# Kernel tuning notes

Measured on AMD Instinct MI355X. Metric: run time of the kernel, lower is better.

Reference implementation:

```python
import jax, jax.numpy as jnp
import numpy as np

B, T, D = 2, 2048, 1024
H, RANK = 16, 32
DH = D // H  # 64


def setup_inputs() -> dict:
    key = jax.random.key(0)
    ks = jax.random.split(key, 6)
    sd = 1.0 / np.sqrt(D)
    sdh = 1.0 / np.sqrt(DH)
    return {
        "x": jax.random.normal(ks[0], (B, T, D), dtype=jnp.float32),
        "W_qkv": jax.random.normal(ks[1], (D, 3 * D), dtype=jnp.float32) * sd,
        "W_q_lsr": jax.random.normal(ks[2], (H, DH, RANK), dtype=jnp.float32) * sdh,
        "W_k_lsr": jax.random.normal(ks[3], (H, DH, RANK), dtype=jnp.float32) * sdh,
        "lsr_core": jnp.ones((H, RANK), dtype=jnp.float32),
        "W_o": jax.random.normal(ks[4], (D, D), dtype=jnp.float32) * sd,
    }


def reference(x, W_qkv, W_q_lsr, W_k_lsr, lsr_core, W_o):
    b, t, d = x.shape
    # Fused QKV projection
    qkv = x @ W_qkv  # (B, T, 3D)
    q, k, v = jnp.split(qkv, 3, axis=-1)
    # (B, H, T, DH)
    q = q.reshape(b, t, H, DH).transpose(0, 2, 1, 3)
    k = k.reshape(b, t, H, DH).transpose(0, 2, 1, 3)
    v = v.reshape(b, t, H, DH).transpose(0, 2, 1, 3)
    # Low-rank bilinear score: q^T Wq diag(core) Wk^T k
    ql = jnp.einsum("bhtd,hdr->bhtr", q, W_q_lsr)  # (B, H, T, R)
    kl = jnp.einsum("bhsd,hdr->bhsr", k, W_k_lsr)  # (B, H, T, R)
    scale = 1.0 / jnp.sqrt(jnp.asarray(RANK, dtype=x.dtype))
    scores = jnp.einsum("bhtr,bhsr->bhts", ql * lsr_core[None, :, None, :], kl) * scale
    # Causal mask
    causal = jnp.tril(jnp.ones((t, t), dtype=bool))
    scores = jnp.where(causal[None, None], scores, jnp.asarray(-jnp.inf, dtype=scores.dtype))
    attn = jax.nn.softmax(scores, axis=-1)
    y = jnp.einsum("bhts,bhsd->bhtd", attn, v)  # (B, H, T, DH)
    y = y.transpose(0, 2, 1, 3).reshape(b, t, d)
    return y @ W_o
```

## Files before the change

kernel.cpp:

```cpp
#include <hip/hip_runtime.h>
#include <hip/hip_bf16.h>

#define B_  2
#define T_  2048
#define D_  1024
#define H_  16
#define DH_ 64
#define R_  32
#define BT_ (B_*T_)
#define BH_ (B_*H_)

typedef unsigned short u16;
typedef unsigned int   u32;
typedef __attribute__((ext_vector_type(8))) short bhalf8;
typedef __attribute__((ext_vector_type(4))) float floatx4;

#define WSB_FLAG  0
#define WSB_XB    256
#define WSB_WCATT (WSB_XB    + 8388608)
#define WSB_QL    (WSB_WCATT + 4194304)
#define WSB_KL    (WSB_QL    + 4194304)
#define WSB_VT    (WSB_KL    + 4194304)
#define WSB_YB    (WSB_VT    + 8388608)
#define WSB_WOT   (WSB_YB    + 8388608)

#define NEG_ -1.0e30f

__device__ __forceinline__ float bfs(u16 s) {
    union { u32 i; float f; } w; w.i = ((u32)s) << 16; return w.f;
}
__device__ __forceinline__ u16 tob(float f) {
    __hip_bfloat16 h = __float2bfloat16(f);
    return *(u16*)&h;
}
__device__ __forceinline__ u32 pack2(float a, float b) {
    return (u32)tob(a) | ((u32)tob(b) << 16);
}

__global__ __launch_bounds__(64) void detect_dtype(const u32* __restrict__ xw,
                                                   int* __restrict__ flag)
{
    const int tid = threadIdx.x;
    int hits = 0;
    for (int i = tid; i < 512; i += 64) {
        const u32 w = xw[i];
        const u32 h = w & 0xFFFFu;
        const u32 e = (h >> 7) & 0xFFu;
        if (h == 0u || (e >= 100u && e <= 150u)) ++hits;
    }
    #pragma unroll
    for (int off = 32; off; off >>= 1) hits += __shfl_down(hits, off, 64);
    if (tid == 0) *flag = (hits >= 300) ? 1 : 0;
}

__global__ __launch_bounds__(256) void convert_x(
    const void* __restrict__ x, u16* __restrict__ xb,
    const int* __restrict__ flag)
{
    const int isbf = *flag;
    const int e = blockIdx.x * 256 + threadIdx.x;
    if (isbf) {
        ((uint4*)xb)[e] = ((const uint4*)x)[e];
    } else {
        float4 a0 = ((const float4*)x)[2*e];
        float4 a1 = ((const float4*)x)[2*e + 1];
        uint4 o;
        o.x = pack2(a0.x, a0.y); o.y = pack2(a0.z, a0.w);
        o.z = pack2(a1.x, a1.y); o.w = pack2(a1.z, a1.w);
        ((uint4*)xb)[e] = o;
    }
}

__global__ __launch_bounds__(256) void fold_mfma(
    const void* __restrict__ Wqkv, const void* __restrict__ Wq_lsr,
    const void* __restrict__ Wk_lsr, const void* __restrict__ core,
    u16* __restrict__ WcatT, const int* __restrict__ flag)
{
    __shared__ __align__(16) u16 Bq[128 * 72];
    __shared__ __align__(16) u16 Bk[128 * 72];
    __shared__ __align__(16) u16 Aq[32 * 72];
    __shared__ __align__(16) u16 Ak[32 * 72];
    const int isbf = *flag;
    const int tid  = threadIdx.x;
    const int lane = tid & 63;
    const int w    = tid >> 6;
    const int n16  = lane & 15;
    const int q4   = lane >> 4;
    const int h    = blockIdx.y;
    const int d0   = blockIdx.x * 128;

    #pragma unroll
    for (int p = 0; p < 8; ++p) {
        const int e  = tid + p * 256;
        const int r  = e & 31, dh = e >> 5;
        float aq, ak;
        if (isbf) {
            aq = bfs(((const u16*)Wq_lsr)[(h*DH_ + dh)*R_ + r]);
            ak = bfs(((const u16*)Wk_lsr)[(h*DH_ + dh)*R_ + r]);
        } else {
            aq = ((const float*)Wq_lsr)[(h*DH_ + dh)*R_ + r];
            ak = ((const float*)Wk_lsr)[(h*DH_ + dh)*R_ + r];
        }
        Aq[r * 72 + dh] = tob(aq);
        Ak[r * 72 + dh] = tob(ak);
    }
    #pragma unroll
    for (int p = 0; p < 8; ++p) {
        const int e  = tid + p * 256;
        const int n  = e >> 4, ch = e & 15;
        if (isbf) {
            uint2 wq = *(const uint2*)((const u16*)Wqkv + (size_t)(d0+n)*(3*D_) + h*DH_ + ch*4);
            uint2 wk = *(const uint2*)((const u16*)Wqkv + (size_t)(d0+n)*(3*D_) + D_ + h*DH_ + ch*4);
            *(uint2*)&Bq[n * 72 + ch*4] = wq;
            *(uint2*)&Bk[n * 72 + ch*4] = wk;
        } else {
            float4 fq = *(const float4*)((const float*)Wqkv + (size_t)(d0+n)*(3*D_) + h*DH_ + ch*4);
            float4 fk = *(const float4*)((const float*)Wqkv + (size_t)(d0+n)*(3*D_) + D_ + h*DH_ + ch*4);
            uint2 oq, ok;
            oq.x = pack2(fq.x, fq.y); oq.y = pack2(fq.z, fq.w);
            ok.x = pack2(fk.x, fk.y); ok.y = pack2(fk.z, fk.w);
            *(uint2*)&Bq[n * 72 + ch*4] = oq;
            *(uint2*)&Bk[n * 72 + ch*4] = ok;
        }
    }
    __syncthreads();

    floatx4 accq[2][2], acck[2][2];
    #pragma unroll
    for (int mi = 0; mi < 2; ++mi)
        #pragma unroll
        for (int ni = 0; ni < 2; ++ni) { accq[mi][ni] = (floatx4)(0.f); acck[mi][ni] = (floatx4)(0.f); }

    #pragma unroll
    for (int kk = 0; kk < 2; ++kk) {
        bhalf8 aqf[2], akf[2], bqf[2], bkf[2];
        #pragma unroll
        for (int mi = 0; mi < 2; ++mi) {
            aqf[mi] = *(const bhalf8*)&Aq[(mi*16 + n16) * 72 + kk*32 + q4*8];
            akf[mi] = *(const bhalf8*)&Ak[(mi*16 + n16) * 72 + kk*32 + q4*8];
        }
        #pragma unroll
        for (int ni = 0; ni < 2; ++ni) {
            bqf[ni] = *(const bhalf8*)&Bq[(w*32 + ni*16 + n16) * 72 + kk*32 + q4*8];
            bkf[ni] = *(const bhalf8*)&Bk[(w*32 + ni*16 + n16) * 72 + kk*32 + q4*8];
        }
        #pragma unroll
        for (int mi = 0; mi < 2; ++mi)
            #pragma unroll
            for (int ni = 0; ni < 2; ++ni) {
                accq[mi][ni] = __builtin_amdgcn_mfma_f32_16x16x32_bf16(aqf[mi], bqf[ni], accq[mi][ni], 0, 0, 0);
                acck[mi][ni] = __builtin_amdgcn_mfma_f32_16x16x32_bf16(akf[mi], bkf[ni], acck[mi][ni], 0, 0, 0);
            }
    }

    const float scale = (float)(0.17677669529663687 * 1.4426950408889634);
    #pragma unroll
    for (int mi = 0; mi < 2; ++mi) {
        #pragma unroll
        for (int rr = 0; rr < 4; ++rr) {
            const int r = mi*16 + q4*4 + rr;
            const float cc = (isbf ? bfs(((const u16*)core)[h*R_ + r])
                                   : ((const float*)core)[h*R_ + r]) * scale;
            #pragma unroll
            for (int ni = 0; ni < 2; ++ni) {
                const int d = d0 + w*32 + ni*16 + n16;
                WcatT[(size_t)(h*R_ + r) * D_ + d]       = tob(accq[mi][ni][rr] * cc);
                WcatT[(size_t)(512 + h*R_ + r) * D_ + d] = tob(acck[mi][ni][rr]);
            }
        }
    }
}

__global__ __launch_bounds__(256) void convert_T(
    const void* __restrict__ src, u16* __restrict__ dst,
    int srcStride, int srcColOff, int dstRowOff, const int* __restrict__ flag)
{
    __shared__ __align__(16) u16 tile[64 * 72];
    const int isbf = *flag;
    const int tid = threadIdx.x;
    const int j0  = blockIdx.x * 64;
    const int i0  = blockIdx.y * 64;
    #pragma unroll
    for (int p = 0; p < 2; ++p) {
        const int e = tid + p * 256;
        const int r = e >> 3, ch = e & 7;
        if (isbf) {
            uint4 w = *(const uint4*)((const u16*)src + (size_t)(i0 + r) * srcStride + srcColOff + j0 + ch*8);
            *(uint4*)&tile[r * 72 + ch*8] = w;
        } else {
            const float* s = (const float*)src + (size_t)(i0 + r) * srcStride + srcColOff + j0 + ch*8;
            float4 a0 = *(const float4*)s;
            float4 a1 = *(const float4*)(s + 4);
            uint4 o;
            o.x = pack2(a0.x, a0.y); o.y = pack2(a0.z, a0.w);
            o.z = pack2(a1.x, a1.y); o.w = pack2(a1.z, a1.w);
            *(uint4*)&tile[r * 72 + ch*8] = o;
        }
    }
    __syncthreads();
    #pragma unroll
    for (int p = 0; p < 2; ++p) {
        const int e = tid + p * 256;
        const int c = e >> 3, ch = e & 7;
        u16 tmp[8];
        #pragma unroll
        for (int j = 0; j < 8; ++j) tmp[j] = tile[(ch*8 + j) * 72 + c];
        *(uint4*)(dst + (size_t)(dstRowOff + j0 + c) * D_ + i0 + ch*8) = *(uint4*)tmp;
    }
}

__global__ __launch_bounds__(256) void gemm1_mfma(
    const u16* __restrict__ xb, const u16* __restrict__ WcatT,
    u16* __restrict__ ql, u16* __restrict__ kl, u16* __restrict__ v_t)
{
    __shared__ __align__(16) u16 As[128 * 72];
    __shared__ __align__(16) u16 Bs[64 * 72];
    const int tid  = threadIdx.x;
    const int lane = tid & 63;
    const int w    = tid >> 6;
    const int n16  = lane & 15;
    const int q4   = lane >> 4;
    const int wx   = w & 1;
    const int wy   = w >> 1;
    const int bm   = blockIdx.y * 128;
    const int bn   = blockIdx.x * 64;

    floatx4 acc[4][2];
    #pragma unroll
    for (int i = 0; i < 4; ++i)
        #pragma unroll
        for (int j = 0; j < 2; ++j) acc[i][j] = (floatx4)(0.f);

    for (int kt = 0; kt < D_; kt += 64) {
        #pragma unroll
        for (int p = 0; p < 4; ++p) {
            const int e = tid + p * 256;
            const int r = e >> 3, ch = (e & 7) * 8;
            *(uint4*)&As[r * 72 + ch] = *(const uint4*)(xb + (size_t)(bm + r) * D_ + kt + ch);
        }
        #pragma unroll
        for (int p = 0; p < 2; ++p) {
            const int e = tid + p * 256;
            const int r = e >> 3, ch = (e & 7) * 8;
            *(uint4*)&Bs[r * 72 + ch] = *(const uint4*)(WcatT + (size_t)(bn + r) * D_ + kt + ch);
        }
        __syncthreads();
        #pragma unroll
        for (int kk = 0; kk < 2; ++kk) {
            bhalf8 a[4], b[2];
            #pragma unroll
            for (int mi = 0; mi < 4; ++mi)
                a[mi] = *(const bhalf8*)&As[(wy*64 + mi*16 + n16) * 72 + kk*32 + q4*8];
            #pragma unroll
            for (int ni = 0; ni < 2; ++ni)
                b[ni] = *(const bhalf8*)&Bs[(wx*32 + ni*16 + n16) * 72 + kk*32 + q4*8];
            #pragma unroll
            for (int mi = 0; mi < 4; ++mi)
                #pragma unroll
                for (int ni = 0; ni < 2; ++ni)
                    acc[mi][ni] = __builtin_amdgcn_mfma_f32_16x16x32_bf16(
                        a[mi], b[ni], acc[mi][ni], 0, 0, 0);
        }
        __syncthreads();
    }

    if (bn < 1024) {
        #pragma unroll
        for (int mi = 0; mi < 4; ++mi) {
            #pragma unroll
            for (int rr = 0; rr < 4; ++rr) {
                const int row = bm + wy*64 + mi*16 + q4*4 + rr;
                const int b   = row >> 11;
                const int t   = row & (T_ - 1);
                #pragma unroll
                for (int ni = 0; ni < 2; ++ni) {
                    const int col = bn + wx*32 + ni*16 + n16;
                    const u16 val = tob(acc[mi][ni][rr]);
                    if (col < 512) {
                        const int h = col >> 5, r = col & 31;
                        ql[((size_t)(b*H_ + h)*T_ + t)*R_ + r] = val;
                    } else {
                        const int c = col - 512; const int h = c >> 5, r = c & 31;
                        kl[((size_t)(b*H_ + h)*T_ + t)*R_ + r] = val;
                    }
                }
            }
        }
    } else {
        #pragma unroll
        for (int mi = 0; mi < 4; ++mi) {
            const int row0 = bm + wy*64 + mi*16 + q4*4;
            const int b = row0 >> 11;
            const int t = row0 & (T_ - 1);
            #pragma unroll
            for (int ni = 0; ni < 2; ++ni) {
                const int c = bn - 1024 + wx*32 + ni*16 + n16;
                const int h = c >> 6, dh = c & 63;
                uint2 o;
                o.x = pack2(acc[mi][ni][0], acc[mi][ni][1]);
                o.y = pack2(acc[mi][ni][2], acc[mi][ni][3]);
                *(uint2*)(v_t + ((size_t)(b*H_ + h) * DH_ + dh) * T_ + t) = o;
            }
        }
    }
}

__global__ __launch_bounds__(256, 3) void attn_kernel(
    const u16* __restrict__ ql, const u16* __restrict__ kl,
    const u16* __restrict__ v_t, u16* __restrict__ y)
{
    __shared__ __align__(16) u16 kls[128 * 40];
    __shared__ __align__(16) u16 vsT[64 * 136];
    __shared__ __align__(16) u16 Ps [4][16][144];

    const int tid  = threadIdx.x;
    const int lane = tid & 63;
    const int w    = tid >> 6;
    const int n16  = lane & 15;
    const int q4   = lane >> 4;
    const int bh   = blockIdx.x;
    const int qt   = 31 - (int)blockIdx.y;
    const int t0   = qt * 64;
    const int nt   = (qt + 2) >> 1;

    const u16* qlb = ql + (size_t)bh * T_ * R_;
    const bhalf8 aq = *(const bhalf8*)(qlb + (size_t)(t0 + w*16 + n16) * R_ + q4*8);

    const u16* klb = kl  + (size_t)bh * T_ * R_;
    const u16* vtb = v_t + (size_t)bh * DH_ * T_;
    const int rk = tid >> 2, ck = (tid & 3) * 8;
    const int dv = tid >> 4, cv = (tid & 15) * 8;

    uint4 kc0 = *(const uint4*)(klb + (size_t)(rk     ) * R_ + ck);
    uint4 kc1 = *(const uint4*)(klb + (size_t)(rk + 64) * R_ + ck);
    uint4 vc0 = *(const uint4*)(vtb + (size_t)(dv     ) * T_ + cv);
    uint4 vc1 = *(const uint4*)(vtb + (size_t)(dv + 16) * T_ + cv);
    uint4 vc2 = *(const uint4*)(vtb + (size_t)(dv + 32) * T_ + cv);
    uint4 vc3 = *(const uint4*)(vtb + (size_t)(dv + 48) * T_ + cv);
    uint4 kn0 = kc0, kn1 = kc1, vn0 = vc0, vn1 = vc1, vn2 = vc2, vn3 = vc3;

    float mrow = NEG_, lrow = 0.f;
    floatx4 O[4];
    #pragma unroll
    for (int c = 0; c < 4; ++c) O[c] = (floatx4)(0.f);

    for (int it = 0; it < nt; ++it) {
        const int s0 = it * 128;
        __syncthreads();
        *(uint4*)&kls[(rk     ) * 40 + ck] = kc0;
        *(uint4*)&kls[(rk + 64) * 40 + ck] = kc1;
        *(uint4*)&vsT[(dv     ) * 136 + cv] = vc0;
        *(uint4*)&vsT[(dv + 16) * 136 + cv] = vc1;
        *(uint4*)&vsT[(dv + 32) * 136 + cv] = vc2;
        *(uint4*)&vsT[(dv + 48) * 136 + cv] = vc3;
        if (it + 1 < nt) {
            const int s1 = s0 + 128;
            kn0 = *(const uint4*)(klb + (size_t)(s1 + rk     ) * R_ + ck);
            kn1 = *(const uint4*)(klb + (size_t)(s1 + rk + 64) * R_ + ck);
            vn0 = *(const uint4*)(vtb + (size_t)(dv     ) * T_ + s1 + cv);
            vn1 = *(const uint4*)(vtb + (size_t)(dv + 16) * T_ + s1 + cv);
            vn2 = *(const uint4*)(vtb + (size_t)(dv + 32) * T_ + s1 + cv);
            vn3 = *(const uint4*)(vtb + (size_t)(dv + 48) * T_ + s1 + cv);
        }
        __syncthreads();

        floatx4 Sc[8];
        #pragma unroll
        for (int c = 0; c < 8; ++c) {
            bhalf8 ak = *(const bhalf8*)&kls[(16*c + n16) * 40 + q4*8];
            Sc[c] = __builtin_amdgcn_mfma_f32_16x16x32_bf16(ak, aq, (floatx4)(0.f), 0, 0, 0);
        }

        if (it == nt - 1) {
            const int tq = w*16 + n16;
            #pragma unroll
            for (int c = 0; c < 8; ++c) {
                const int sb = s0 - t0 + 16*c + 4*q4;
                #pragma unroll
                for (int r = 0; r < 4; ++r)
                    if (sb + r > tq) Sc[c][r] = NEG_;
            }
        }

        float cmax[8];
        #pragma unroll
        for (int c = 0; c < 8; ++c)
            cmax[c] = fmaxf(fmaxf(Sc[c][0], Sc[c][1]), fmaxf(Sc[c][2], Sc[c][3]));
        float rmax = fmaxf(fmaxf(fmaxf(cmax[0], cmax[1]), fmaxf(cmax[2], cmax[3])),
                           fmaxf(fmaxf(cmax[4], cmax[5]), fmaxf(cmax[6], cmax[7])));
        rmax = fmaxf(rmax, __shfl_xor(rmax, 16, 64));
        rmax = fmaxf(rmax, __shfl_xor(rmax, 32, 64));

        const float mn = fmaxf(mrow, rmax);
        const int norescale = __all(rmax <= mrow);

        float csum[8];
        #pragma unroll
        for (int c = 0; c < 8; ++c) {
            #pragma unroll
            for (int r = 0; r < 4; ++r)
                Sc[c][r] = __builtin_amdgcn_exp2f(Sc[c][r] - mn);
            csum[c] = (Sc[c][0] + Sc[c][1]) + (Sc[c][2] + Sc[c][3]);
        }
        float rsum = ((csum[0] + csum[1]) + (csum[2] + csum[3]))
                   + ((csum[4] + csum[5]) + (csum[6] + csum[7]));
        rsum += __shfl_xor(rsum, 16, 64);
        rsum += __shfl_xor(rsum, 32, 64);

        if (norescale) {
            lrow += rsum;
        } else {
            const float alpha = __builtin_amdgcn_exp2f(mrow - mn);
            mrow = mn;
            lrow = lrow * alpha + rsum;
            float aO[4];
            #pragma unroll
            for (int r = 0; r < 4; ++r) aO[r] = __shfl(alpha, q4*4 + r, 64);
            #pragma unroll
            for (int c2 = 0; c2 < 4; ++c2)
                #pragma unroll
                for (int r = 0; r < 4; ++r) O[c2][r] *= aO[r];
        }

        #pragma unroll
        for (int c = 0; c < 8; ++c) {
            uint2 pw;
            pw.x = pack2(Sc[c][0], Sc[c][1]);
            pw.y = pack2(Sc[c][2], Sc[c][3]);
            *(uint2*)&Ps[w][n16][16*c + 4*q4] = pw;
        }

        #pragma unroll
        for (int kc = 0; kc < 4; ++kc) {
            bhalf8 pa = *(const bhalf8*)&Ps[w][n16][kc*32 + q4*8];
            #pragma unroll
            for (int c2 = 0; c2 < 4; ++c2) {
                bhalf8 bv = *(const bhalf8*)&vsT[(16*c2 + n16) * 136 + kc*32 + q4*8];
                O[c2] = __builtin_amdgcn_mfma_f32_16x16x32_bf16(pa, bv, O[c2], 0, 0, 0);
            }
        }

        kc0 = kn0; kc1 = kn1; vc0 = vn0; vc1 = vn1; vc2 = vn2; vc3 = vn3;
    }

    const int b = bh >> 4, h = bh & 15;
    float lb[4];
    #pragma unroll
    for (int r = 0; r < 4; ++r) lb[r] = __shfl(lrow, q4*4 + r, 64);
    #pragma unroll
    for (int r = 0; r < 4; ++r) {
        const float rl = 1.0f / lb[r];
        const int t = t0 + w*16 + q4*4 + r;
        #pragma unroll
        for (int c2 = 0; c2 < 4; ++c2)
            y[((size_t)b * T_ + t) * D_ + h * DH_ + 16*c2 + n16] = tob(O[c2][r] * rl);
    }
}

__global__ __launch_bounds__(256) void out_gemm_mfma(
    const u16* __restrict__ yb, const u16* __restrict__ WoT,
    float* __restrict__ out)
{
    __shared__ __align__(16) u16 As[128 * 72];
    __shared__ __align__(16) u16 Bs[64 * 72];
    const int tid  = threadIdx.x;
    const int lane = tid & 63;
    const int w    = tid >> 6;
    const int n16  = lane & 15;
    const int q4   = lane >> 4;
    const int wx   = w & 1;
    const int wy   = w >> 1;
    const int bm   = blockIdx.y * 128;
    const int bn   = blockIdx.x * 64;

    floatx4 acc[4][2];
    #pragma unroll
    for (int i = 0; i < 4; ++i)
        #pragma unroll
        for (int j = 0; j < 2; ++j) acc[i][j] = (floatx4)(0.f);

    for (int kt = 0; kt < D_; kt += 64) {
        #pragma unroll
        for (int p = 0; p < 4; ++p) {
            const int e = tid + p * 256;
            const int r = e >> 3, ch = (e & 7) * 8;
            *(uint4*)&As[r * 72 + ch] = *(const uint4*)(yb + (size_t)(bm + r) * D_ + kt + ch);
        }
        #pragma unroll
        for (int p = 0; p < 2; ++p) {
            const int e = tid + p * 256;
            const int r = e >> 3, ch = (e & 7) * 8;
            *(uint4*)&Bs[r * 72 + ch] = *(const uint4*)(WoT + (size_t)(bn + r) * D_ + kt + ch);
        }
        __syncthreads();
        #pragma unroll
        for (int kk = 0; kk < 2; ++kk) {
            bhalf8 a[4], b[2];
            #pragma unroll
            for (int mi = 0; mi < 4; ++mi)
                a[mi] = *(const bhalf8*)&As[(wy*64 + mi*16 + n16) * 72 + kk*32 + q4*8];
            #pragma unroll
            for (int ni = 0; ni < 2; ++ni)
                b[ni] = *(const bhalf8*)&Bs[(wx*32 + ni*16 + n16) * 72 + kk*32 + q4*8];
            #pragma unroll
            for (int mi = 0; mi < 4; ++mi)
                #pragma unroll
                for (int ni = 0; ni < 2; ++ni)
                    acc[mi][ni] = __builtin_amdgcn_mfma_f32_16x16x32_bf16(
                        a[mi], b[ni], acc[mi][ni], 0, 0, 0);
        }
        __syncthreads();
    }

    #pragma unroll
    for (int mi = 0; mi < 4; ++mi) {
        #pragma unroll
        for (int rr = 0; rr < 4; ++rr) {
            const int row = bm + wy*64 + mi*16 + q4*4 + rr;
            #pragma unroll
            for (int ni = 0; ni < 2; ++ni) {
                const int col = bn + wx*32 + ni*16 + n16;
                out[(size_t)row * D_ + col] = acc[mi][ni][rr];
            }
        }
    }
}

extern "C" void kernel_launch(void* const* d_in, const int* in_sizes, int n_in,
                              void* d_out, int out_size, void* d_ws, size_t ws_size,
                              hipStream_t stream)
{
    (void)out_size; (void)ws_size;
    const void* in_x = nullptr; const void* in_wqkv = nullptr;
    const void* in_wq = nullptr; const void* in_wk = nullptr;
    const void* in_core = nullptr; const void* in_wo = nullptr;
    for (int i = 0; i < n_in; ++i) {
        const int s = in_sizes[i];
        if      (s == BT_*D_)     { if (!in_x)    in_x    = d_in[i]; }
        else if (s == D_*3*D_)    { if (!in_wqkv) in_wqkv = d_in[i]; }
        else if (s == H_*DH_*R_)  { if (!in_wq)   in_wq   = d_in[i]; else if (!in_wk) in_wk = d_in[i]; }
        else if (s == H_*R_)      { if (!in_core) in_core = d_in[i]; }
        else if (s == D_*D_)      { if (!in_wo)   in_wo   = d_in[i]; }
    }
    if (!in_x)    in_x    = d_in[0];
    if (!in_wqkv) in_wqkv = d_in[1];
    if (!in_wq)   in_wq   = d_in[2];
    if (!in_wk)   in_wk   = d_in[3];
    if (!in_core) in_core = d_in[4];
    if (!in_wo)   in_wo   = d_in[5];

    float* out = (float*)d_out;

    char* ws    = (char*)d_ws;
    int*  flag  = (int*)(ws + WSB_FLAG);
    u16*  xb    = (u16*)(ws + WSB_XB);
    u16*  WcatT = (u16*)(ws + WSB_WCATT);
    u16*  ql    = (u16*)(ws + WSB_QL);
    u16*  kl    = (u16*)(ws + WSB_KL);
    u16*  v_t   = (u16*)(ws + WSB_VT);
    u16*  yb    = (u16*)(ws + WSB_YB);
    u16*  WoT   = (u16*)(ws + WSB_WOT);

    detect_dtype<<<1, 64, 0, stream>>>((const u32*)in_x, flag);
    convert_x<<<2048, 256, 0, stream>>>(in_x, xb, flag);
    fold_mfma<<<dim3(8, 16), 256, 0, stream>>>(in_wqkv, in_wq, in_wk, in_core, WcatT, flag);
    convert_T<<<dim3(16,16), 256, 0, stream>>>(in_wqkv, WcatT, 3*D_, 2*D_, 1024, flag);
    convert_T<<<dim3(16,16), 256, 0, stream>>>(in_wo,   WoT,   D_,   0,    0,    flag);
    gemm1_mfma<<<dim3(32, 32), 256, 0, stream>>>(xb, WcatT, ql, kl, v_t);
    attn_kernel<<<dim3(32, 32), 256, 0, stream>>>(ql, kl, v_t, yb);
    out_gemm_mfma<<<dim3(16, 32), 256, 0, stream>>>(yb, WoT, out);
}
```

Measured before the change: 189.0 us.

## Keep softmax probabilities in registers by permuting V shared-memory layout

The attention kernel no longer routes the bf16 probability tile through a per-warp shared buffer. Each lane packs its own score accumulators straight into the MFMA A operand, and V^T is written to shared memory with a permuted column order so the key dimension lines up with that register layout. This removes an LDS write/read round trip and frees shared memory, so the launch bound is raised from 3 to 4 blocks per CU. In exchange, the V stores become narrower 8-byte writes, and correctness depends on the permutation exactly matching the MFMA lane mapping.

```diff
diff --git a/kernel.cpp b/kernel.cpp
--- a/kernel.cpp
+++ b/kernel.cpp
@@ -305,13 +305,12 @@
     }
 }
 
-__global__ __launch_bounds__(256, 3) void attn_kernel(
+__global__ __launch_bounds__(256, 4) void attn_kernel(
     const u16* __restrict__ ql, const u16* __restrict__ kl,
     const u16* __restrict__ v_t, u16* __restrict__ y)
 {
     __shared__ __align__(16) u16 kls[128 * 40];
     __shared__ __align__(16) u16 vsT[64 * 136];
-    __shared__ __align__(16) u16 Ps [4][16][144];
 
     const int tid  = threadIdx.x;
     const int lane = tid & 63;
@@ -329,7 +328,10 @@
     const u16* klb = kl  + (size_t)bh * T_ * R_;
     const u16* vtb = v_t + (size_t)bh * DH_ * T_;
     const int rk = tid >> 2, ck = (tid & 3) * 8;
-    const int dv = tid >> 4, cv = (tid & 15) * 8;
+    const int dv = tid >> 4;
+    const int m  = tid & 15;
+    const int cv = m * 8;
+    const int pb = ((m & 1) << 4) | (((m >> 1) & 1) << 2) | ((m >> 2) << 5);
 
     uint4 kc0 = *(const uint4*)(klb + (size_t)(rk     ) * R_ + ck);
     uint4 kc1 = *(const uint4*)(klb + (size_t)(rk + 64) * R_ + ck);
@@ -349,10 +351,17 @@
         __syncthreads();
         *(uint4*)&kls[(rk     ) * 40 + ck] = kc0;
         *(uint4*)&kls[(rk + 64) * 40 + ck] = kc1;
-        *(uint4*)&vsT[(dv     ) * 136 + cv] = vc0;
-        *(uint4*)&vsT[(dv + 16) * 136 + cv] = vc1;
-        *(uint4*)&vsT[(dv + 32) * 136 + cv] = vc2;
-        *(uint4*)&vsT[(dv + 48) * 136 + cv] = vc3;
+        {
+            uint2 t;
+            t.x = vc0.x; t.y = vc0.y; *(uint2*)&vsT[(dv     ) * 136 + pb    ] = t;
+            t.x = vc0.z; t.y = vc0.w; *(uint2*)&vsT[(dv     ) * 136 + pb + 8] = t;
+            t.x = vc1.x; t.y = vc1.y; *(uint2*)&vsT[(dv + 16) * 136 + pb    ] = t;
+            t.x = vc1.z; t.y = vc1.w; *(uint2*)&vsT[(dv + 16) * 136 + pb + 8] = t;
+            t.x = vc2.x; t.y = vc2.y; *(uint2*)&vsT[(dv + 32) * 136 + pb    ] = t;
+            t.x = vc2.z; t.y = vc2.w; *(uint2*)&vsT[(dv + 32) * 136 + pb + 8] = t;
+            t.x = vc3.x; t.y = vc3.y; *(uint2*)&vsT[(dv + 48) * 136 + pb    ] = t;
+            t.x = vc3.z; t.y = vc3.w; *(uint2*)&vsT[(dv + 48) * 136 + pb + 8] = t;
+        }
         if (it + 1 < nt) {
             const int s1 = s0 + 128;
             kn0 = *(const uint4*)(klb + (size_t)(s1 + rk     ) * R_ + ck);
@@ -423,16 +432,13 @@
         }
 
         #pragma unroll
-        for (int c = 0; c < 8; ++c) {
-            uint2 pw;
-            pw.x = pack2(Sc[c][0], Sc[c][1]);
-            pw.y = pack2(Sc[c][2], Sc[c][3]);
-            *(uint2*)&Ps[w][n16][16*c + 4*q4] = pw;
-        }
-
-        #pragma unroll
         for (int kc = 0; kc < 4; ++kc) {
-            bhalf8 pa = *(const bhalf8*)&Ps[w][n16][kc*32 + q4*8];
+            union { u32 wd[4]; bhalf8 v; } pu;
+            pu.wd[0] = pack2(Sc[2*kc    ][0], Sc[2*kc    ][1]);
+            pu.wd[1] = pack2(Sc[2*kc    ][2], Sc[2*kc    ][3]);
+            pu.wd[2] = pack2(Sc[2*kc + 1][0], Sc[2*kc + 1][1]);
+            pu.wd[3] = pack2(Sc[2*kc + 1][2], Sc[2*kc + 1][3]);
+            const bhalf8 pa = pu.v;
             #pragma unroll
             for (int c2 = 0; c2 < 4; ++c2) {
                 bhalf8 bv = *(const bhalf8*)&vsT[(16*c2 + n16) * 136 + kc*32 + q4*8];
```

New measurement: 189.5 us. No clear change (+0.3%).
